# Performance work log

Hardware: AMD Instinct MI355X
Metric: run time of the kernel (lower is better)

Reference implementation:

```python
import jax, jax.numpy as jnp
import numpy as np

B, N, F_ATOM, F_BOND = 128, 128, 64, 16
HIDDEN, OUT = 512, 128


def setup_inputs() -> dict:
    key = jax.random.key(0)
    ks = jax.random.split(key, 7)
    atom_feats = jax.random.normal(ks[0], (B, N, F_ATOM), dtype=jnp.float32)
    bond_feats = jax.random.normal(ks[1], (B, N, N, F_BOND), dtype=jnp.float32)
    adj_matrix = (jax.random.uniform(ks[2], (B, N, N)) < 0.15).astype(jnp.float32)
    fan1 = 1.0 / np.sqrt(2 * F_ATOM + F_BOND)
    fan2 = 1.0 / np.sqrt(HIDDEN)
    W1 = jax.random.normal(ks[3], (2 * F_ATOM + F_BOND, HIDDEN), dtype=jnp.float32) * fan1
    b1 = jnp.zeros((HIDDEN,), dtype=jnp.float32)
    W2 = jax.random.normal(ks[4], (HIDDEN, OUT), dtype=jnp.float32) * fan2
    b2 = jnp.zeros((OUT,), dtype=jnp.float32)
    return {"atom_feats": atom_feats, "bond_feats": bond_feats, "adj_matrix": adj_matrix,
            "W1": W1, "b1": b1, "W2": W2, "b2": b2}


def reference(atom_feats, bond_feats, adj_matrix, W1, b1, W2, b2):
    # Original: expanded[b,i,j,f] = atom_feats[b,j,f]; cat with bond_feats;
    # mask by adj[b,i,j]; sum over dim=1 (i). Equivalent fused math:
    #   atom part : sum_i adj[b,i,j] * atom[b,j,f] = atom[b,j,f] * colsum(adj)[b,j]
    #   bond part : sum_i adj[b,i,j] * bond[b,i,j,f]
    deg = jnp.sum(adj_matrix, axis=1)                       # [B,N] column sums
    agg_atom = atom_feats * deg[..., None]                  # [B,N,F_atom]
    agg_bond = jnp.einsum('bij,bijf->bjf', adj_matrix, bond_feats)  # [B,N,F_bond]
    h = jnp.concatenate([atom_feats, agg_atom, agg_bond], axis=-1)  # [B,N,2Fa+Fb]
    h = jax.nn.relu(h @ W1 + b1)                            # [B,N,HIDDEN]
    return (h @ W2 + b2).sum(axis=1)                        # [B,OUT]
```

## Files before the change

### kernel.cpp

```cpp
#include <hip/hip_runtime.h>
#include <hip/hip_bf16.h>

#define B_   128
#define N_   128
#define FA   64
#define FB   16
#define K1   144
#define KP   160
#define HID  512
#define OUT_ 128

typedef __attribute__((ext_vector_type(8))) short short8;
typedef __attribute__((ext_vector_type(4))) float f32x4;

__device__ __forceinline__ ushort f2b(float v) {
  __hip_bfloat16 h = __float2bfloat16(v);
  return *reinterpret_cast<ushort*>(&h);
}
__device__ __forceinline__ float4 add4(float4 a, float4 b) {
  return make_float4(a.x + b.x, a.y + b.y, a.z + b.z, a.w + b.w);
}

__global__ __launch_bounds__(512) void k_prep_agg(
    const float* __restrict__ atom, const float* __restrict__ bond,
    const float* __restrict__ adj, const float* __restrict__ W1,
    ushort* __restrict__ w1f, ushort* __restrict__ hinf,
    float* __restrict__ out) {
  const int t = threadIdx.x;

  if (blockIdx.x < 20) {
    const int U  = blockIdx.x * 512 + t;
    const int c  = U & 15;
    const int g  = (U >> 4) & 3;
    const int t5 = U >> 6;
    const int ks = t5 % 5;
    const int ntg = t5 / 5;
    const int n  = ntg * 16 + c;
    const int k0 = ks * 32 + g * 8;
    short8 v;
#pragma unroll
    for (int e = 0; e < 8; ++e) {
      const int k = k0 + e;
      v[e] = (short)f2b((k < K1) ? W1[k * HID + n] : 0.f);
    }
    reinterpret_cast<short8*>(w1f)[U] = v;
    return;
  }
  if (blockIdx.x == 20) {
    float4* o4 = reinterpret_cast<float4*>(out);
    for (int u = t; u < B_ * OUT_ / 4; u += 512)
      o4[u] = make_float4(0.f, 0.f, 0.f, 0.f);
    return;
  }

  const int bid = blockIdx.x - 21;
  const int b  = bid >> 3;
  const int m  = bid & 7;
  const int j0 = m * 16;

  __shared__ float  sAdj[N_][16];
  __shared__ ushort sList[16][N_];
  __shared__ int    sCnt[16];
  __shared__ float4 sPart[16][4][8];
  __shared__ ushort sRow[16][KP];

  const float* adjb = adj + (size_t)b * N_ * N_ + j0;
  for (int u = t; u < N_ * 4; u += 512) {
    const int i = u >> 2, q = u & 3;
    *reinterpret_cast<float4*>(&sAdj[i][q * 4]) =
        *reinterpret_cast<const float4*>(&adjb[(size_t)i * N_ + q * 4]);
  }
  __syncthreads();

  const int wv = t >> 6, l = t & 63;
#pragma unroll
  for (int q = 0; q < 2; ++q) {
    const int jj = wv * 2 + q;
    const float a0 = sAdj[l][jj];
    const float a1 = sAdj[l + 64][jj];
    const unsigned long long m0 = __ballot(a0 != 0.f);
    const unsigned long long m1 = __ballot(a1 != 0.f);
    const int c0 = __popcll(m0);
    unsigned int p0 = __builtin_amdgcn_mbcnt_lo((unsigned)m0, 0u);
    p0 = __builtin_amdgcn_mbcnt_hi((unsigned)(m0 >> 32), p0);
    if (a0 != 0.f) sList[jj][p0] = (ushort)l;
    unsigned int p1 = __builtin_amdgcn_mbcnt_lo((unsigned)m1, 0u);
    p1 = __builtin_amdgcn_mbcnt_hi((unsigned)(m1 >> 32), p1);
    if (a1 != 0.f) sList[jj][c0 + p1] = (ushort)(l + 64);
    if (l == 0) sCnt[jj] = c0 + __popcll(m1);
  }
  __syncthreads();

  {
    const int fq = t & 3;
    const int is = (t >> 2) & 7;
    const int jl = t >> 5;
    const int cnt = sCnt[jl];
    const float4* bp4 = reinterpret_cast<const float4*>(
        bond + ((size_t)b * N_ * N_ + (j0 + jl)) * FB) + fq;
    float4 a0 = {0,0,0,0}, a1 = {0,0,0,0};
    int e = is;
    for (; e + 8 < cnt; e += 16) {
      const int i0 = sList[jl][e];
      const int i1 = sList[jl][e + 8];
      a0 = add4(a0, bp4[(size_t)i0 * 512]);
      a1 = add4(a1, bp4[(size_t)i1 * 512]);
    }
    for (; e < cnt; e += 8) a0 = add4(a0, bp4[(size_t)sList[jl][e] * 512]);
    sPart[jl][fq][is] = add4(a0, a1);
  }
  __syncthreads();

  if (t < 256) {
    const int f  = t & 15;
    const int jl = t >> 4;
    const float* pc = reinterpret_cast<const float*>(&sPart[jl][f >> 2][0]);
    const int c3 = f & 3;
    const float aggv = (((pc[c3] + pc[4 + c3]) + (pc[8 + c3] + pc[12 + c3])) +
                        ((pc[16 + c3] + pc[20 + c3]) +
                         (pc[24 + c3] + pc[28 + c3])));
    const float deg = (float)sCnt[jl];
    const float* ab = atom + ((size_t)b * N_ + j0 + jl) * FA;
    for (int c = f; c < FA; c += 16) {
      const float av = ab[c];
      sRow[jl][c]      = f2b(av);
      sRow[jl][FA + c] = f2b(av * deg);
    }
    sRow[jl][2 * FA + f] = f2b(aggv);
    sRow[jl][K1 + f]     = 0;
  }
  __syncthreads();

  uint4* dst = reinterpret_cast<uint4*>(hinf) + (size_t)(b * 8 + m) * 320;
  for (int u = t; u < 320; u += 512) {
    const int s = u >> 4, j2 = u & 15;
    const int ks = s >> 2, g = s & 3;
    dst[ks * 64 + g * 16 + j2] =
        *reinterpret_cast<const uint4*>(&sRow[j2][s * 8]);
  }
}

__global__ __launch_bounds__(512) void k_gemm_out(
    const ushort* __restrict__ hinf, const ushort* __restrict__ w1f,
    const float* __restrict__ b1, const float* __restrict__ W2,
    const float* __restrict__ b2, float* __restrict__ out) {
  const int b  = blockIdx.x >> 1;
  const int nh = blockIdx.x & 1;
  const int t  = threadIdx.x;
  const int w  = t >> 6;
  const int l  = t & 63;

  __shared__ ushort sA[40 * 512];
  __shared__ float  sS[256];
  __shared__ float  sRed[4][128];

  const uint4* g4 = reinterpret_cast<const uint4*>(hinf) + (size_t)b * 2560;
  uint4* s4 = reinterpret_cast<uint4*>(sA);
  for (int u = t; u < 2560; u += 512) s4[u] = g4[u];

  const int n0 = nh * 256 + w * 32;
  const short8* w8 = reinterpret_cast<const short8*>(w1f);
  short8 bfrag[2][5];
#pragma unroll
  for (int nt = 0; nt < 2; ++nt) {
    const int ntg = (n0 >> 4) + nt;
#pragma unroll
    for (int ks = 0; ks < 5; ++ks)
      bfrag[nt][ks] = w8[(ntg * 5 + ks) * 64 + l];
  }
  float bias[2];
#pragma unroll
  for (int nt = 0; nt < 2; ++nt) bias[nt] = b1[n0 + nt * 16 + (l & 15)];

  __syncthreads();

  const short8* a8 = reinterpret_cast<const short8*>(sA);
  float cs[2] = {0.f, 0.f};
  for (int m = 0; m < 8; ++m) {
    short8 af[5];
#pragma unroll
    for (int ks = 0; ks < 5; ++ks) af[ks] = a8[(m * 5 + ks) * 64 + l];
#pragma unroll
    for (int nt = 0; nt < 2; ++nt) {
      f32x4 acc = {0.f, 0.f, 0.f, 0.f};
#pragma unroll
      for (int ks = 0; ks < 5; ++ks)
        acc = __builtin_amdgcn_mfma_f32_16x16x32_bf16(af[ks], bfrag[nt][ks],
                                                      acc, 0, 0, 0);
      float p = 0.f;
#pragma unroll
      for (int r = 0; r < 4; ++r) p += fmaxf(acc[r] + bias[nt], 0.f);
      cs[nt] += p;
    }
  }

#pragma unroll
  for (int nt = 0; nt < 2; ++nt) {
    float v = cs[nt];
    v += __shfl_xor(v, 16);
    v += __shfl_xor(v, 32);
    if ((l >> 4) == 0) sS[w * 32 + nt * 16 + (l & 15)] = v;
  }
  __syncthreads();

  const int o = t & 127, kq = t >> 7;
  const float* W2p = W2 + (size_t)(nh * 256 + kq * 64) * OUT_ + o;
  float acc = 0.f;
#pragma unroll 8
  for (int k = 0; k < 64; ++k) acc += sS[kq * 64 + k] * W2p[(size_t)k * OUT_];
  sRed[kq][o] = acc;
  __syncthreads();
  if (kq == 0) {
    float v = (sRed[0][o] + sRed[1][o]) + (sRed[2][o] + sRed[3][o]);
    if (nh == 0) v += (float)N_ * b2[o];
    atomicAdd(&out[b * OUT_ + o], v);
  }
}

extern "C" void kernel_launch(void* const* d_in, const int* in_sizes, int n_in,
                              void* d_out, int out_size, void* d_ws, size_t ws_size,
                              hipStream_t stream) {
  const float* atom = (const float*)d_in[0];
  const float* bond = (const float*)d_in[1];
  const float* adj  = (const float*)d_in[2];
  const float* W1   = (const float*)d_in[3];
  const float* b1   = (const float*)d_in[4];
  const float* W2   = (const float*)d_in[5];
  const float* b2   = (const float*)d_in[6];
  float* out = (float*)d_out;

  ushort* hinf = (ushort*)d_ws;
  ushort* w1f  = hinf + (size_t)B_ * 2560 * 8;

  k_prep_agg<<<21 + B_ * 8, 512, 0, stream>>>(atom, bond, adj, W1, w1f, hinf,
                                              out);
  k_gemm_out<<<B_ * 2, 512, 0, stream>>>(hinf, w1f, b1, W2, b2, out);
}
```

Measured before the change: 26.51 us.

## Restructure bond aggregation to row-chunked edge lists with LDS atomics over 64 columns

Each aggregation block now covers 64 destination columns instead of 16, so the grid shrinks from 1024 to 256 blocks. Adjacency is walked in 32-row chunks, building a flat edge list with a prefix scan. Bond vectors are gathered per edge and accumulated through shared-memory float atomics into a transposed buffer. The aim is better load balance across edges and more contiguous bond reads, at the cost of many more barriers, LDS atomic contention and fewer blocks to fill the GPU.

```diff
diff --git a/kernel.cpp b/kernel.cpp
--- a/kernel.cpp
+++ b/kernel.cpp
@@ -16,9 +16,6 @@
 __device__ __forceinline__ ushort f2b(float v) {
   __hip_bfloat16 h = __float2bfloat16(v);
   return *reinterpret_cast<ushort*>(&h);
-}
-__device__ __forceinline__ float4 add4(float4 a, float4 b) {
-  return make_float4(a.x + b.x, a.y + b.y, a.z + b.z, a.w + b.w);
 }
 
 __global__ __launch_bounds__(512) void k_prep_agg(
@@ -54,89 +51,156 @@
   }
 
   const int bid = blockIdx.x - 21;
-  const int b  = bid >> 3;
-  const int m  = bid & 7;
-  const int j0 = m * 16;
-
-  __shared__ float  sAdj[N_][16];
-  __shared__ ushort sList[16][N_];
-  __shared__ int    sCnt[16];
-  __shared__ float4 sPart[16][4][8];
-  __shared__ ushort sRow[16][KP];
-
+  const int b  = bid >> 1;
+  const int h  = bid & 1;
+  const int j0 = h * 64;
+  const int wv = t >> 6, l = t & 63;
+
+  __shared__ float  sAdj[32][64];
+  __shared__ unsigned long long sMask[32];
+  __shared__ int    sCnt[32], sOff[32], sTotal;
+  __shared__ ushort sList[2048];
+  __shared__ float  sAggT[16][64];
+  __shared__ float  sDegP[8][64];
+  __shared__ ushort sRow[64][KP];
+
+  for (int u = t; u < 16 * 64; u += 512) ((float*)sAggT)[u] = 0.f;
+
+  int degloc = 0;
   const float* adjb = adj + (size_t)b * N_ * N_ + j0;
-  for (int u = t; u < N_ * 4; u += 512) {
-    const int i = u >> 2, q = u & 3;
-    *reinterpret_cast<float4*>(&sAdj[i][q * 4]) =
-        *reinterpret_cast<const float4*>(&adjb[(size_t)i * N_ + q * 4]);
-  }
-  __syncthreads();
-
-  const int wv = t >> 6, l = t & 63;
-#pragma unroll
-  for (int q = 0; q < 2; ++q) {
-    const int jj = wv * 2 + q;
-    const float a0 = sAdj[l][jj];
-    const float a1 = sAdj[l + 64][jj];
-    const unsigned long long m0 = __ballot(a0 != 0.f);
-    const unsigned long long m1 = __ballot(a1 != 0.f);
-    const int c0 = __popcll(m0);
-    unsigned int p0 = __builtin_amdgcn_mbcnt_lo((unsigned)m0, 0u);
-    p0 = __builtin_amdgcn_mbcnt_hi((unsigned)(m0 >> 32), p0);
-    if (a0 != 0.f) sList[jj][p0] = (ushort)l;
-    unsigned int p1 = __builtin_amdgcn_mbcnt_lo((unsigned)m1, 0u);
-    p1 = __builtin_amdgcn_mbcnt_hi((unsigned)(m1 >> 32), p1);
-    if (a1 != 0.f) sList[jj][c0 + p1] = (ushort)(l + 64);
-    if (l == 0) sCnt[jj] = c0 + __popcll(m1);
+
+  for (int ic = 0; ic < 4; ++ic) {
+    const int i0 = ic * 32;
+    __syncthreads();
+
+    {
+      const int i = t >> 4, q = t & 15;
+      *reinterpret_cast<float4*>(&sAdj[i][q * 4]) =
+          *reinterpret_cast<const float4*>(&adjb[(size_t)(i0 + i) * N_ + q * 4]);
+    }
+    __syncthreads();
+
+#pragma unroll
+    for (int q = 0; q < 4; ++q) {
+      const int il = wv * 4 + q;
+      const float a = sAdj[il][l];
+      const unsigned long long mk = __ballot(a != 0.f);
+      degloc += (a != 0.f) ? 1 : 0;
+      if (l == 0) { sMask[il] = mk; sCnt[il] = __popcll(mk); }
+    }
+    __syncthreads();
+
+    if (wv == 0 && l < 32) {
+      const int c = sCnt[l];
+      int inc = c;
+      for (int d = 1; d < 32; d <<= 1) {
+        const int u = __shfl_up(inc, d);
+        if (l >= d) inc += u;
+      }
+      sOff[l] = inc - c;
+      if (l == 31) sTotal = inc;
+    }
+    __syncthreads();
+
+#pragma unroll
+    for (int q = 0; q < 4; ++q) {
+      const int il = wv * 4 + q;
+      const unsigned long long mk = sMask[il];
+      if ((mk >> l) & 1ull) {
+        unsigned int p = __builtin_amdgcn_mbcnt_lo((unsigned)mk, 0u);
+        p = __builtin_amdgcn_mbcnt_hi((unsigned)(mk >> 32), p);
+        sList[sOff[il] + p] = (ushort)((il << 6) | l);
+      }
+    }
+    __syncthreads();
+
+    {
+      const int E  = sTotal;
+      const int fq = t & 3;
+      const int s0 = t >> 2;
+      const float4* bp4 = reinterpret_cast<const float4*>(bond) +
+          (((size_t)b * N_ + i0) * N_ + j0) * 4 + fq;
+      for (int base = 0; base < E; base += 512) {
+        const int sA2 = base + s0, sB = sA2 + 128, sC = sA2 + 256, sD = sA2 + 384;
+        int e0 = (sA2 < E) ? sList[sA2] : -1;
+        int e1 = (sB  < E) ? sList[sB]  : -1;
+        int e2 = (sC  < E) ? sList[sC]  : -1;
+        int e3 = (sD  < E) ? sList[sD]  : -1;
+        float4 v0, v1, v2, v3;
+        if (e0 >= 0) v0 = bp4[(size_t)((e0 >> 6) * N_ + (e0 & 63)) * 4];
+        if (e1 >= 0) v1 = bp4[(size_t)((e1 >> 6) * N_ + (e1 & 63)) * 4];
+        if (e2 >= 0) v2 = bp4[(size_t)((e2 >> 6) * N_ + (e2 & 63)) * 4];
+        if (e3 >= 0) v3 = bp4[(size_t)((e3 >> 6) * N_ + (e3 & 63)) * 4];
+        const int f0 = fq * 4;
+        if (e0 >= 0) {
+          atomicAdd(&sAggT[f0 + 0][e0 & 63], v0.x);
+          atomicAdd(&sAggT[f0 + 1][e0 & 63], v0.y);
+          atomicAdd(&sAggT[f0 + 2][e0 & 63], v0.z);
+          atomicAdd(&sAggT[f0 + 3][e0 & 63], v0.w);
+        }
+        if (e1 >= 0) {
+          atomicAdd(&sAggT[f0 + 0][e1 & 63], v1.x);
+          atomicAdd(&sAggT[f0 + 1][e1 & 63], v1.y);
+          atomicAdd(&sAggT[f0 + 2][e1 & 63], v1.z);
+          atomicAdd(&sAggT[f0 + 3][e1 & 63], v1.w);
+        }
+        if (e2 >= 0) {
+          atomicAdd(&sAggT[f0 + 0][e2 & 63], v2.x);
+          atomicAdd(&sAggT[f0 + 1][e2 & 63], v2.y);
+          atomicAdd(&sAggT[f0 + 2][e2 & 63], v2.z);
+          atomicAdd(&sAggT[f0 + 3][e2 & 63], v2.w);
+        }
+        if (e3 >= 0) {
+          atomicAdd(&sAggT[f0 + 0][e3 & 63], v3.x);
+          atomicAdd(&sAggT[f0 + 1][e3 & 63], v3.y);
+          atomicAdd(&sAggT[f0 + 2][e3 & 63], v3.z);
+          atomicAdd(&sAggT[f0 + 3][e3 & 63], v3.w);
+        }
+      }
+    }
+  }
+
+  sDegP[wv][l] = (float)degloc;
+  __syncthreads();
+  if (t < 64) {
+    float d = 0.f;
+#pragma unroll
+    for (int w2 = 0; w2 < 8; ++w2) d += sDegP[w2][t];
+    sDegP[0][t] = d;
   }
   __syncthreads();
 
   {
-    const int fq = t & 3;
-    const int is = (t >> 2) & 7;
-    const int jl = t >> 5;
-    const int cnt = sCnt[jl];
-    const float4* bp4 = reinterpret_cast<const float4*>(
-        bond + ((size_t)b * N_ * N_ + (j0 + jl)) * FB) + fq;
-    float4 a0 = {0,0,0,0}, a1 = {0,0,0,0};
-    int e = is;
-    for (; e + 8 < cnt; e += 16) {
-      const int i0 = sList[jl][e];
-      const int i1 = sList[jl][e + 8];
-      a0 = add4(a0, bp4[(size_t)i0 * 512]);
-      a1 = add4(a1, bp4[(size_t)i1 * 512]);
-    }
-    for (; e < cnt; e += 8) a0 = add4(a0, bp4[(size_t)sList[jl][e] * 512]);
-    sPart[jl][fq][is] = add4(a0, a1);
-  }
-  __syncthreads();
-
-  if (t < 256) {
-    const int f  = t & 15;
-    const int jl = t >> 4;
-    const float* pc = reinterpret_cast<const float*>(&sPart[jl][f >> 2][0]);
-    const int c3 = f & 3;
-    const float aggv = (((pc[c3] + pc[4 + c3]) + (pc[8 + c3] + pc[12 + c3])) +
-                        ((pc[16 + c3] + pc[20 + c3]) +
-                         (pc[24 + c3] + pc[28 + c3])));
-    const float deg = (float)sCnt[jl];
-    const float* ab = atom + ((size_t)b * N_ + j0 + jl) * FA;
-    for (int c = f; c < FA; c += 16) {
-      const float av = ab[c];
-      sRow[jl][c]      = f2b(av);
-      sRow[jl][FA + c] = f2b(av * deg);
-    }
-    sRow[jl][2 * FA + f] = f2b(aggv);
+    const int jl = t >> 3;
+    const int fo = (t & 7) * 8;
+    const float deg = sDegP[0][jl];
+    const float* ab = atom + ((size_t)b * N_ + j0 + jl) * FA + fo;
+    const float4 av0 = *reinterpret_cast<const float4*>(ab);
+    const float4 av1 = *reinterpret_cast<const float4*>(ab + 4);
+    const float av[8] = {av0.x, av0.y, av0.z, av0.w, av1.x, av1.y, av1.z, av1.w};
+#pragma unroll
+    for (int c2 = 0; c2 < 8; ++c2) {
+      sRow[jl][fo + c2]      = f2b(av[c2]);
+      sRow[jl][FA + fo + c2] = f2b(av[c2] * deg);
+    }
+  }
+  for (int u = t; u < 64 * 16; u += 512) {
+    const int jl = u >> 4, f = u & 15;
+    sRow[jl][2 * FA + f] = f2b(sAggT[f][jl]);
     sRow[jl][K1 + f]     = 0;
   }
   __syncthreads();
 
-  uint4* dst = reinterpret_cast<uint4*>(hinf) + (size_t)(b * 8 + m) * 320;
-  for (int u = t; u < 320; u += 512) {
-    const int s = u >> 4, j2 = u & 15;
+  uint4* dstb = reinterpret_cast<uint4*>(hinf) + (size_t)(b * 8 + h * 4) * 320;
+  for (int u = t; u < 4 * 320; u += 512) {
+    const int mt = u >> 8 >> 2;
+    const int mt2 = u / 320;
+    const int r = u - mt2 * 320;
+    const int s = r >> 4, j2 = r & 15;
     const int ks = s >> 2, g = s & 3;
-    dst[ks * 64 + g * 16 + j2] =
-        *reinterpret_cast<const uint4*>(&sRow[j2][s * 8]);
+    (void)mt;
+    dstb[(size_t)mt2 * 320 + ks * 64 + g * 16 + j2] =
+        *reinterpret_cast<const uint4*>(&sRow[mt2 * 16 + j2][s * 8]);
   }
 }
 
@@ -232,7 +296,7 @@
   ushort* hinf = (ushort*)d_ws;
   ushort* w1f  = hinf + (size_t)B_ * 2560 * 8;
 
-  k_prep_agg<<<21 + B_ * 8, 512, 0, stream>>>(atom, bond, adj, W1, w1f, hinf,
+  k_prep_agg<<<21 + B_ * 2, 512, 0, stream>>>(atom, bond, adj, W1, w1f, hinf,
                                               out);
   k_gemm_out<<<B_ * 2, 512, 0, stream>>>(hinf, w1f, b1, W2, b2, out);
 }
```

Measured after the change: 50.23 us. +89.5%, slower.
